# Kernel tuning notes

Hardware: AMD Instinct MI355X
Metric: run time of the kernel (lower is better)

The kernel has to match this reference:

```python
import jax, jax.numpy as jnp
import numpy as np
import math

N, E, D, H = 50000, 1600000, 128, 8
DH = D // H  # per-head dim
EPS = 1e-5   # batchnorm eps


def _attn(q_in, k_in, v_in, Wq, Wk, Wv, src, dst):
    # GAT-style edge attention: score = exp(clip(<K[src],Q[dst]>/sqrt(DH), -5, 5))
    Q = (q_in @ Wq.T).reshape(-1, H, DH)
    K = (k_in @ Wk.T).reshape(-1, H, DH)
    V = (v_in @ Wv.T).reshape(-1, H, DH)
    score = jnp.exp(jnp.clip((K[src] * Q[dst]).sum(-1) / math.sqrt(DH), -5.0, 5.0))  # [E,H]
    wV = jax.ops.segment_sum(V[src] * score[:, :, None], dst, num_segments=N)  # [N,H,DH]
    z = jax.ops.segment_sum(score, dst, num_segments=N)                         # [N,H]
    return (wV / z[:, :, None]).reshape(-1, D)


def _bn(x, gamma, beta):
    # BatchNorm1d in training mode: biased batch stats over nodes
    m = x.mean(0)
    v = x.var(0)
    return (x - m) / jnp.sqrt(v + EPS) * gamma + beta


def setup_inputs() -> dict:
    key = jax.random.key(0)
    ks = iter(jax.random.split(key, 48))

    def w(shape, scale=None):
        s = scale if scale is not None else 1.0 / math.sqrt(shape[-1])
        return jax.random.normal(next(ks), shape, jnp.float32) * s

    inp = dict(
        h=w((N, D), 1.0),
        sv=w((N, D), 1.0),
        src=jax.random.randint(next(ks), (E,), 0, N, jnp.int32),
        dst=jax.random.randint(next(ks), (E,), 0, N, jnp.int32),
    )
    for nm in ["Wq_sv", "Wk_sv", "Wv_sv", "Wq_cv", "Wk_cv", "Wv_cv",
               "Wq_sh", "Wk_sh", "Wv_sh"]:
        inp[nm] = w((D, D))
    inp.update(
        Wo=w((D, 2 * D)), bo=jnp.zeros((D,), jnp.float32),
        Wo_h=w((D, 2 * D)), bo_h=jnp.zeros((D,), jnp.float32),
        W1=w((2 * D, D)), b1=jnp.zeros((2 * D,), jnp.float32),
        W2=w((D, 2 * D)), b2=jnp.zeros((D,), jnp.float32),
        W1h=w((2 * D, D)), b1h=jnp.zeros((2 * D,), jnp.float32),
        W2h=w((D, 2 * D)), b2h=jnp.zeros((D,), jnp.float32),
        Wg1=w((D, D)), bg1=jnp.zeros((D,), jnp.float32),
        Wg2=w((D, D)), bg2=jnp.zeros((D,), jnp.float32),
        gbn1=jnp.ones((D,), jnp.float32), bbn1=jnp.zeros((D,), jnp.float32),
        gbn2=jnp.ones((D,), jnp.float32), bbn2=jnp.zeros((D,), jnp.float32),
        gbn1h=jnp.ones((D,), jnp.float32), bbn1h=jnp.zeros((D,), jnp.float32),
        gbn2h=jnp.ones((D,), jnp.float32), bbn2h=jnp.zeros((D,), jnp.float32),
    )
    return inp


def reference(h, sv, src, dst,
              Wq_sv, Wk_sv, Wv_sv, Wq_cv, Wk_cv, Wv_cv, Wq_sh, Wk_sh, Wv_sh,
              Wo, bo, Wo_h, bo_h,
              W1, b1, W2, b2, W1h, b1h, W2h, b2h,
              Wg1, bg1, Wg2, bg2,
              gbn1, bbn1, gbn2, bbn2, gbn1h, bbn1h, gbn2h, bbn2h):
    h_in1, sv_in1 = h, sv
    # --- h branch ---
    a_self = _attn(h, h, h, Wq_sv, Wk_sv, Wv_sv, src, dst)
    a_cross = _attn(h, sv, sv, Wq_cv, Wk_cv, Wv_cv, src, dst)
    hO = jnp.concatenate([a_self, a_cross], -1) @ Wo.T + bo
    h1 = _bn(h_in1 + hO, gbn1, bbn1)
    ffn = jax.nn.relu(h1 @ W1.T + b1) @ W2.T + b2
    h_out = _bn(h1 + ffn, gbn2, bbn2)
    # --- state-vector branch ---
    a_self_h = _attn(sv, sv, sv, Wq_sh, Wk_sh, Wv_sh, src, dst)
    # faithful to source: cross_attention_v weights reused here
    a_cross_h = _attn(sv, h_in1, h_in1, Wq_cv, Wk_cv, Wv_cv, src, dst)
    svO = jnp.concatenate([a_self_h, a_cross_h], -1) @ Wo_h.T + bo_h
    g1 = jax.nn.sigmoid(h_in1 @ Wg1.T + bg1)
    sv1 = _bn((1.0 - g1) * sv_in1 + g1 * svO, gbn1h, bbn1h)
    ffn_h = jax.nn.relu(sv1 @ W1h.T + b1h) @ W2h.T + b2h
    g2 = jax.nn.sigmoid(h_in1 @ Wg2.T + bg2)
    sv_out = _bn((1.0 - g2) * sv1 + g2 * ffn_h, gbn2h, bbn2h)
    return (h_out, sv_out)
```

## Files before the change

### kernel.cpp

```cpp
#include <hip/hip_runtime.h>

typedef _Float16 f16x8 __attribute__((ext_vector_type(8)));
typedef _Float16 f16x2 __attribute__((ext_vector_type(2)));
typedef __fp16 fp16x2_raw __attribute__((ext_vector_type(2)));
typedef float f32x4 __attribute__((ext_vector_type(4)));
typedef float f32x2 __attribute__((ext_vector_type(2)));
typedef unsigned int uint32;
typedef unsigned short ushort16;
typedef unsigned char uchar;

#define EPS_BN 1e-5f

__device__ __forceinline__ uint32 pk16(float a, float b){
  fp16x2_raw h = __builtin_amdgcn_cvt_pkrtz(a, b);
  return *(uint32*)&h;
}
__device__ __forceinline__ uchar f2fp8(float f){
  uint32 p = __builtin_amdgcn_cvt_pk_fp8_f32(f, f, 0, false);
  return (uchar)(p & 0xff);
}
__device__ __forceinline__ f32x2 fp8pair_lo(uint32 w){
  return __builtin_amdgcn_cvt_pk_f32_fp8(w, false);
}
__device__ __forceinline__ f32x2 fp8pair_hi(uint32 w){
  return __builtin_amdgcn_cvt_pk_f32_fp8(w, true);
}

struct WEnt { const float* s; const float* s2; ushort16* d; int KD, MD, nfrag; };
struct WConv { WEnt e[16]; };

__global__ __launch_bounds__(256) void conv_w_k(WConv a){
  WEnt t = a.e[blockIdx.y];
  int fid = blockIdx.x * 256 + threadIdx.x;
  if (fid >= t.nfrag) return;
  int lane = fid & 63, sm = fid >> 6;
  int MT = t.MD >> 4;
  int s = sm / MT, m = sm - s * MT;
  int row = m * 16 + (lane & 15);
  int col = s * 32 + (lane >> 4) * 8;
  const float* sp = t.s;
  if (t.s2 && row >= 128){ sp = t.s2; row -= 128; }
  const float* p = sp + (size_t)row * t.KD + col;
  uint4 o;
  o.x = pk16(p[0], p[1]); o.y = pk16(p[2], p[3]);
  o.z = pk16(p[4], p[5]); o.w = pk16(p[6], p[7]);
  *(uint4*)(t.d + (size_t)fid * 8) = o;
}

__global__ __launch_bounds__(256) void conv2h_k(const float* __restrict__ a, const float* __restrict__ b,
                                                ushort16* __restrict__ da, ushort16* __restrict__ db, int n,
                                                const int* __restrict__ dst, int* __restrict__ cnt, int E){
  if (blockIdx.y < 2){
    const float* s = blockIdx.y ? b : a;
    ushort16* d = blockIdx.y ? db : da;
    int i = (blockIdx.x * 256 + threadIdx.x) * 4;
    if (i >= n) return;
    float4 v = *(const float4*)(s + i);
    uint2 p;
    p.x = pk16(v.x, v.y);
    p.y = pk16(v.z, v.w);
    *(uint2*)(d + i) = p;
  } else {
    int i = blockIdx.x * 256 + threadIdx.x;
    int stride = gridDim.x * 256;
    for (; i < E; i += stride) atomicAdd(&cnt[dst[i]], 1);
  }
}

__global__ __launch_bounds__(256) void scan_part_k(const int* __restrict__ cnt, int* __restrict__ bsum, int N){
  int tid = threadIdx.x, lane = tid & 63, wv = tid >> 6;
  int base = blockIdx.x * 1024 + tid * 4;
  int ts = 0;
  #pragma unroll
  for (int j = 0; j < 4; j++) if (base + j < N) ts += cnt[base + j];
  #pragma unroll
  for (int d = 1; d < 64; d <<= 1) ts += __shfl_xor(ts, d);
  __shared__ int wt[4];
  if (lane == 0) wt[wv] = ts;
  __syncthreads();
  if (tid == 0) bsum[blockIdx.x] = wt[0] + wt[1] + wt[2] + wt[3];
}

__global__ __launch_bounds__(256) void scan_out_k(const int* __restrict__ cnt, const int* __restrict__ bsum,
                                                  int* __restrict__ row_off, int* __restrict__ cursor,
                                                  int* __restrict__ bcur,
                                                  int N, int E, int shift){
  int tid = threadIdx.x, lane = tid & 63, wv = tid >> 6;
  int bp = 0;
  for (int i = lane; i < (int)blockIdx.x; i += 64) bp += bsum[i];
  #pragma unroll
  for (int d = 1; d < 64; d <<= 1) bp += __shfl_xor(bp, d);
  int base = blockIdx.x * 1024 + tid * 4;
  int c[4]; int ts = 0;
  #pragma unroll
  for (int j = 0; j < 4; j++){ c[j] = (base + j < N) ? cnt[base + j] : 0; ts += c[j]; }
  int inc = ts;
  #pragma unroll
  for (int d = 1; d < 64; d <<= 1){
    int t = __shfl_up(inc, d);
    if (lane >= d) inc += t;
  }
  int wexcl = inc - ts;
  __shared__ int wt[4];
  if (lane == 63) wt[wv] = inc;
  __syncthreads();
  int woff = 0;
  for (int w = 0; w < 4; w++) if (w < wv) woff += wt[w];
  int off = bp + woff + wexcl;
  int mask = (1 << shift) - 1;
  #pragma unroll
  for (int j = 0; j < 4; j++){
    int d = base + j;
    if (d < N){
      row_off[d] = off; cursor[d] = off;
      if ((d & mask) == 0) bcur[d >> shift] = off;
      off += c[j];
    }
  }
  if (blockIdx.x == 0 && tid == 0) row_off[N] = E;
}

#define BIN_TB 512
#define BIN_TILE 4096
__global__ __launch_bounds__(512) void bin_k(const int* __restrict__ src, const int* __restrict__ dst,
                                             int* __restrict__ bcur, uint2* __restrict__ ebuf,
                                             int E, int shift, int B){
  __shared__ int lhist[128];
  __shared__ int lstart[128];
  __shared__ int gbase[128];
  __shared__ uint2 lpair[BIN_TILE];
  int tid = threadIdx.x;
  int base = blockIdx.x * BIN_TILE;
  int cnt = E - base; if (cnt > BIN_TILE) cnt = BIN_TILE;
  if (tid < 128) lhist[tid] = 0;
  __syncthreads();
  int myb[8], myrank[8];
  uint2 myp[8];
  int nmine = 0;
  #pragma unroll
  for (int j = 0; j < 8; j++){
    int i = tid + j * BIN_TB;
    if (i < cnt){
      int s = src[base + i], d = dst[base + i];
      int b = d >> shift;
      myp[nmine] = make_uint2((uint32)s, (uint32)d);
      myb[nmine] = b;
      myrank[nmine] = atomicAdd(&lhist[b], 1);
      nmine++;
    }
  }
  __syncthreads();
  if (tid == 0){
    int run = 0;
    for (int b = 0; b < B; b++){ lstart[b] = run; run += lhist[b]; }
  }
  __syncthreads();
  if (tid < B) gbase[tid] = atomicAdd(&bcur[tid], lhist[tid]);
  for (int j = 0; j < nmine; j++){
    lpair[lstart[myb[j]] + myrank[j]] = myp[j];
  }
  __syncthreads();
  for (int i = tid; i < cnt; i += BIN_TB){
    uint2 p = lpair[i];
    int b = (int)(p.y >> shift);
    ebuf[gbase[b] + (i - lstart[b])] = p;
  }
}

#define BF_SPLIT 8
__global__ __launch_bounds__(256) void bfill_k(const uint2* __restrict__ ebuf, const int* __restrict__ row_off,
                                               int* __restrict__ cursor, int* __restrict__ esrc,
                                               int shift, int N){
  int b = blockIdx.x / BF_SPLIT, slice = blockIdx.x % BF_SPLIT;
  int d0 = b << shift;
  int d1 = (b + 1) << shift; if (d1 > N) d1 = N;
  if (d0 >= N) return;
  int e0 = row_off[d0], e1 = row_off[d1];
  for (int i = e0 + slice * 256 + (int)threadIdx.x; i < e1; i += 256 * BF_SPLIT){
    uint2 p = ebuf[i];
    int pos = atomicAdd(&cursor[p.y], 1);
    esrc[pos] = (int)p.x;
  }
}

struct QkvArgs {
  const ushort16* Xq[4];
  const ushort16* Xkv[4];
  const ushort16* Wq[4];
  const ushort16* Wk[4];
  const ushort16* Wv[4];
  ushort16* Qo[4];
};
__global__ __launch_bounds__(256) void gemm_qkv_k(
    QkvArgs A, uchar* __restrict__ KV8, int N)
{
  __shared__ _Float16 Qs[4][16 * 136];
  __shared__ uchar Ks[4][16 * 136];
  __shared__ uchar Vs[4][16 * 136];
  int slot = blockIdx.y;
  int toff = slot << 8;
  const ushort16* Xq = A.Xq[slot];
  const ushort16* Xkv = A.Xkv[slot];
  ushort16* Qo = A.Qo[slot];
  int lane = threadIdx.x & 63, wv = threadIdx.x >> 6;
  int l15 = lane & 15, kq = lane >> 4;
  int rowbase = (blockIdx.x * 4 + wv) * 16;
  int row = rowbase + l15;
  int rc = row < N ? row : N - 1;
  const f16x8* aq = (const f16x8*)(Xq + (size_t)rc * 128 + kq * 8);
  const f16x8* ak = (const f16x8*)(Xkv + (size_t)rc * 128 + kq * 8);
  f16x8 Aq[4], Ak[4];
  #pragma unroll
  for (int s = 0; s < 4; s++){ Aq[s] = aq[s * 4]; Ak[s] = ak[s * 4]; }
  const f16x8* Wqf = (const f16x8*)A.Wq[slot];
  const f16x8* Wkf = (const f16x8*)A.Wk[slot];
  const f16x8* Wvf = (const f16x8*)A.Wv[slot];
  f32x4 q[8], k[8], v[8];
  #pragma unroll
  for (int m = 0; m < 8; m++){ q[m] = (f32x4)(0.f); k[m] = (f32x4)(0.f); v[m] = (f32x4)(0.f); }
  #pragma unroll
  for (int s = 0; s < 4; s++){
    #pragma unroll
    for (int m = 0; m < 8; m++){
      int fi = (s * 8 + m) * 64 + lane;
      q[m] = __builtin_amdgcn_mfma_f32_16x16x32_f16(Aq[s], Wqf[fi], q[m], 0, 0, 0);
      k[m] = __builtin_amdgcn_mfma_f32_16x16x32_f16(Ak[s], Wkf[fi], k[m], 0, 0, 0);
      v[m] = __builtin_amdgcn_mfma_f32_16x16x32_f16(Ak[s], Wvf[fi], v[m], 0, 0, 0);
    }
  }
  #pragma unroll
  for (int m = 0; m < 8; m++){
    int col = m * 16 + l15;
    #pragma unroll
    for (int r = 0; r < 4; r++){
      int lrow = kq * 4 + r;
      Qs[wv][lrow * 136 + col] = (_Float16)q[m][r];
      Ks[wv][lrow * 136 + col] = f2fp8(k[m][r]);
      Vs[wv][lrow * 136 + col] = f2fp8(v[m][r]);
    }
  }
  #pragma unroll
  for (int p = 0; p < 4; p++){
    int lrow = p * 4 + (lane >> 4);
    int rr = rowbase + lrow;
    int col8 = l15 * 8;
    if (rr < N){
      uint4 qv = *(uint4*)&Qs[wv][lrow * 136 + col8];
      *(uint4*)(Qo + (size_t)rr * 128 + col8) = qv;
      uint2 kv = *(uint2*)&Ks[wv][lrow * 136 + col8];
      *(uint2*)(KV8 + (size_t)rr * 1024 + toff + col8) = kv;
      uint2 vv = *(uint2*)&Vs[wv][lrow * 136 + col8];
      *(uint2*)(KV8 + (size_t)rr * 1024 + toff + 128 + col8) = vv;
    }
  }
}

template<int KD, int MD, int EPI, int ABN, int ST, int GS>
__device__ __forceinline__ void gemm_body(
    const ushort16* __restrict__ X, const ushort16* __restrict__ W,
    const float* __restrict__ bias, const float* __restrict__ bias2,
    const ushort16* __restrict__ resb, const ushort16* __restrict__ gatep,
    const float* __restrict__ rstats, const float* __restrict__ rg, const float* __restrict__ rb,
    const float* __restrict__ astats, const float* __restrict__ ag, const float* __restrict__ ab,
    ushort16* __restrict__ outb, float* __restrict__ stats_out, int N, float invN,
    _Float16* OsBase, float* sstB, float* sst2B)
{
  constexpr int KS = KD / 32;
  constexpr int MT = MD / 16;
  constexpr int LSTR = MD + 8;
  int lane = threadIdx.x & 63, wv = threadIdx.x >> 6;
  _Float16* OsW = OsBase + wv * 16 * LSTR;
  int l15 = lane & 15, kq = lane >> 4;
  int rowbase = (blockIdx.x * 4 + wv) * 16;
  int row = rowbase + l15;
  int rc = row < N ? row : N - 1;
  const f16x8* ap = (const f16x8*)(X + (size_t)rc * KD + kq * 8);
  f16x8 a[KS];
  #pragma unroll
  for (int s = 0; s < KS; s++) a[s] = ap[s * 4];
  if constexpr (ABN){
    #pragma unroll
    for (int s = 0; s < KS; s++){
      #pragma unroll
      for (int j = 0; j < 8; j++){
        int c = s * 32 + kq * 8 + j;
        float mm = astats[c] * invN;
        float var = astats[128 + c] * invN - mm * mm;
        float rs = rsqrtf(var + EPS_BN);
        float scc = rs * ag[c];
        float shh = ab[c] - mm * scc;
        a[s][j] = (_Float16)((float)a[s][j] * scc + shh);
      }
    }
  }
  const f16x8* Wf = (const f16x8*)W;
  f32x4 acc[MT];
  #pragma unroll
  for (int m = 0; m < MT; m++) acc[m] = (f32x4)(0.f);
  #pragma unroll
  for (int s = 0; s < KS; s++){
    #pragma unroll
    for (int m = 0; m < MT; m++){
      acc[m] = __builtin_amdgcn_mfma_f32_16x16x32_f16(a[s], Wf[(s * MT + m) * 64 + lane], acc[m], 0, 0, 0);
    }
  }
  float ps[MT], ps2[MT];
  if constexpr (ST){
    #pragma unroll
    for (int m = 0; m < MT; m++){ ps[m] = 0.f; ps2[m] = 0.f; }
  }
  int r0 = rowbase + kq * 4;
  #pragma unroll
  for (int m = 0; m < MT; m++){
    int col = m * 16 + l15;
    float bv;
    if (bias2 && col >= 128) bv = bias2[col - 128];
    else bv = bias[col];
    float sc = 0.f, sh = 0.f;
    if constexpr (EPI == 5 || EPI == 6){
      float mm = rstats[col] * invN;
      float var = rstats[128 + col] * invN - mm * mm;
      float rs = rsqrtf(var + EPS_BN);
      sc = rs * rg[col]; sh = rb[col] - mm * sc;
    }
    #pragma unroll
    for (int r = 0; r < 4; r++){
      int rr = r0 + r;
      float v;
      {
        int rrc = rr < N ? rr : N - 1;
        v = acc[m][r] + bv;
        if constexpr (EPI == 1) v = fmaxf(v, 0.f);
        if constexpr (EPI == 2) v = 1.f / (1.f + __expf(-v));
        if constexpr (EPI == 3){
          union { ushort16 u; _Float16 h; } cv; cv.u = resb[(size_t)rrc * 128 + col];
          v += (float)cv.h;
        }
        if constexpr (EPI == 5){
          union { ushort16 u; _Float16 h; } cv; cv.u = resb[(size_t)rrc * 128 + col];
          v += (float)cv.h * sc + sh;
        }
        if constexpr (EPI == 4 || EPI == 6){
          union { ushort16 u; _Float16 h; } gv; gv.u = gatep[(size_t)rrc * GS + col];
          union { ushort16 u; _Float16 h; } cv; cv.u = resb[(size_t)rrc * 128 + col];
          float g = (float)gv.h;
          float rv = (float)cv.h;
          if constexpr (EPI == 6) rv = rv * sc + sh;
          v = (1.f - g) * rv + g * v;
        }
      }
      OsW[(kq * 4 + r) * LSTR + col] = (_Float16)v;
      if constexpr (ST){
        if (rr < N){ ps[m] += v; ps2[m] += v * v; }
      }
    }
  }
  if constexpr (MD == 128){
    #pragma unroll
    for (int p = 0; p < 4; p++){
      int lrow = p * 4 + (lane >> 4);
      int rr = rowbase + lrow;
      int col8 = l15 * 8;
      if (rr < N){
        uint4 ov = *(uint4*)&OsW[lrow * LSTR + col8];
        *(uint4*)(outb + (size_t)rr * MD + col8) = ov;
      }
    }
  } else {
    #pragma unroll
    for (int p = 0; p < 8; p++){
      int lrow = p * 2 + (lane >> 5);
      int rr = rowbase + lrow;
      int col8 = (lane & 31) * 8;
      if (rr < N){
        uint4 ov = *(uint4*)&OsW[lrow * LSTR + col8];
        *(uint4*)(outb + (size_t)rr * MD + col8) = ov;
      }
    }
  }
  if constexpr (ST){
    #pragma unroll
    for (int m = 0; m < MT; m++){
      float s = ps[m], s2 = ps2[m];
      s  += __shfl_xor(s, 16);  s  += __shfl_xor(s, 32);
      s2 += __shfl_xor(s2, 16); s2 += __shfl_xor(s2, 32);
      if (lane < 16){ sstB[wv * 128 + m * 16 + l15] = s; sst2B[wv * 128 + m * 16 + l15] = s2; }
    }
    __syncthreads();
    int tid = threadIdx.x;
    if (tid < 128){
      atomicAdd(&stats_out[tid], sstB[tid] + sstB[128 + tid] + sstB[256 + tid] + sstB[384 + tid]);
    } else {
      int c = tid - 128;
      atomicAdd(&stats_out[tid], sst2B[c] + sst2B[128 + c] + sst2B[256 + c] + sst2B[384 + c]);
    }
  }
}

template<int KD, int MD, int EPI, int ABN, int ST, int GS>
__global__ __launch_bounds__(256) void gemm_k(
    const ushort16* __restrict__ X, const ushort16* __restrict__ W,
    const float* __restrict__ bias, const float* __restrict__ bias2,
    const ushort16* __restrict__ resb, const ushort16* __restrict__ gatep,
    const float* __restrict__ rstats, const float* __restrict__ rg, const float* __restrict__ rb,
    const float* __restrict__ astats, const float* __restrict__ ag, const float* __restrict__ ab,
    ushort16* __restrict__ outb, float* __restrict__ stats_out, int N, float invN)
{
  __shared__ _Float16 Os[4 * 16 * (MD + 8)];
  __shared__ float sst[512];
  __shared__ float sst2[512];
  gemm_body<KD, MD, EPI, ABN, ST, GS>(X, W, bias, bias2, resb, gatep, rstats, rg, rb,
                                      astats, ag, ab, outb, stats_out, N, invN, Os, sst, sst2);
}

struct GPairArgs {
  const ushort16* X[2]; const ushort16* W[2];
  const float* bias[2];
  const ushort16* resb[2]; const ushort16* gatep[2];
  const float* rstats[2]; const float* rg[2]; const float* rb[2];
  const float* astats[2]; const float* ag[2]; const float* ab[2];
  ushort16* outb[2]; float* stats_out[2];
};
template<int KD, int MD, int EPI0, int EPI1, int ABN, int ST, int GS>
__global__ __launch_bounds__(256) void gemm_pair_k(GPairArgs A, int N, float invN)
{
  __shared__ _Float16 Os[4 * 16 * (MD + 8)];
  __shared__ float sst[512];
  __shared__ float sst2[512];
  int y = blockIdx.y;
  if (y == 0){
    gemm_body<KD, MD, EPI0, ABN, ST, GS>(A.X[0], A.W[0], A.bias[0], nullptr, A.resb[0], A.gatep[0],
        A.rstats[0], A.rg[0], A.rb[0], A.astats[0], A.ag[0], A.ab[0],
        A.outb[0], A.stats_out[0], N, invN, Os, sst, sst2);
  } else {
    gemm_body<KD, MD, EPI1, ABN, ST, GS>(A.X[1], A.W[1], A.bias[1], nullptr, A.resb[1], A.gatep[1],
        A.rstats[1], A.rg[1], A.rb[1], A.astats[1], A.ag[1], A.ab[1],
        A.outb[1], A.stats_out[1], N, invN, Os, sst, sst2);
  }
}

__global__ __launch_bounds__(256) void attn4_k(
    const ushort16* __restrict__ Qa, const ushort16* __restrict__ Qb,
    const ushort16* __restrict__ Qc, const ushort16* __restrict__ Qd,
    const uchar* __restrict__ KV,
    const int* __restrict__ row_off, const int* __restrict__ esrc,
    ushort16* __restrict__ cat_h, ushort16* __restrict__ cat_sv, int N)
{
  int wv = threadIdx.x >> 6, lane = threadIdx.x & 63;
  int n = blockIdx.x * 4 + wv;
  if (n >= N) return;
  int g = lane >> 4, j = lane & 15;
  uint32 j8 = (uint32)j * 8u;
  const float QS = 0.25f * 1.44269504088896f;
  const float CL = 7.21347520444482f;
  const ushort16* Qp[4] = {Qa, Qb, Qc, Qd};
  f32x2 q[4][4];
  #pragma unroll
  for (int t = 0; t < 4; t++){
    uint4 u = *(const uint4*)(Qp[t] + (size_t)n * 128 + j8);
    f16x2 h0 = *(f16x2*)&u.x, h1 = *(f16x2*)&u.y;
    f16x2 h2 = *(f16x2*)&u.z, h3 = *(f16x2*)&u.w;
    q[t][0].x = (float)h0.x * QS; q[t][0].y = (float)h0.y * QS;
    q[t][1].x = (float)h1.x * QS; q[t][1].y = (float)h1.y * QS;
    q[t][2].x = (float)h2.x * QS; q[t][2].y = (float)h2.y * QS;
    q[t][3].x = (float)h3.x * QS; q[t][3].y = (float)h3.y * QS;
  }
  int e0 = row_off[n], e1 = row_off[n + 1];
  int itmax = (e1 - e0 + 3) >> 2;
  f32x2 ac[4][4];
  #pragma unroll
  for (int t = 0; t < 4; t++){
    #pragma unroll
    for (int r = 0; r < 4; r++) ac[t][r] = (f32x2)(0.f);
  }
  float z[4] = {0.f, 0.f, 0.f, 0.f};
  int e = e0 + g;
  int s = (e < e1) ? esrc[e] : -1;
  uint32 off = ((uint32)(s < 0 ? 0 : s) << 10) + j8;
  uint2 kc[4], vc[4];
  #pragma unroll
  for (int t = 0; t < 4; t++){
    kc[t] = *(const uint2*)(KV + off + t * 256);
    vc[t] = *(const uint2*)(KV + off + t * 256 + 128);
  }
  for (int it = 0; it < itmax; ++it){
    int e2 = e + 4;
    int s2 = (e2 < e1) ? esrc[e2] : -1;
    uint32 off2 = ((uint32)(s2 < 0 ? 0 : s2) << 10) + j8;
    uint2 kn[4], vn[4];
    #pragma unroll
    for (int t = 0; t < 4; t++){
      kn[t] = *(const uint2*)(KV + off2 + t * 256);
      vn[t] = *(const uint2*)(KV + off2 + t * 256 + 128);
    }
    if (s >= 0){
      #pragma unroll
      for (int t = 0; t < 4; t++){
        f32x2 k0 = fp8pair_lo(kc[t].x), k1 = fp8pair_hi(kc[t].x);
        f32x2 k2 = fp8pair_lo(kc[t].y), k3 = fp8pair_hi(kc[t].y);
        f32x2 dd = k0 * q[t][0] + k1 * q[t][1] + k2 * q[t][2] + k3 * q[t][3];
        float d = dd.x + dd.y;
        d += __shfl_xor(d, 1);
        float sc = __builtin_amdgcn_exp2f(__builtin_amdgcn_fmed3f(d, -CL, CL));
        f32x2 v0 = fp8pair_lo(vc[t].x), v1 = fp8pair_hi(vc[t].x);
        f32x2 v2 = fp8pair_lo(vc[t].y), v3 = fp8pair_hi(vc[t].y);
        f32x2 sv; sv.x = sc; sv.y = sc;
        ac[t][0] += sv * v0; ac[t][1] += sv * v1;
        ac[t][2] += sv * v2; ac[t][3] += sv * v3;
        z[t] += sc;
      }
    }
    e = e2; s = s2; off = off2;
    #pragma unroll
    for (int t = 0; t < 4; t++){ kc[t] = kn[t]; vc[t] = vn[t]; }
  }
  #pragma unroll
  for (int t = 0; t < 4; t++){
    #pragma unroll
    for (int r = 0; r < 4; r++){
      ac[t][r].x += __shfl_xor(ac[t][r].x, 16);
      ac[t][r].y += __shfl_xor(ac[t][r].y, 16);
      ac[t][r].x += __shfl_xor(ac[t][r].x, 32);
      ac[t][r].y += __shfl_xor(ac[t][r].y, 32);
    }
    z[t] += __shfl_xor(z[t], 16);
    z[t] += __shfl_xor(z[t], 32);
  }
  if (g == 0){
    size_t base = (size_t)n * 256 + j8;
    #pragma unroll
    for (int t = 0; t < 4; t++){
      float rz = __builtin_amdgcn_rcpf(z[t]);
      uint4 o;
      o.x = pk16(ac[t][0].x * rz, ac[t][0].y * rz);
      o.y = pk16(ac[t][1].x * rz, ac[t][1].y * rz);
      o.z = pk16(ac[t][2].x * rz, ac[t][2].y * rz);
      o.w = pk16(ac[t][3].x * rz, ac[t][3].y * rz);
      ushort16* dp = (t < 2) ? cat_h : cat_sv;
      *(uint4*)(dp + base + (t & 1) * 128) = o;
    }
  }
}

struct Bn2Args {
  const ushort16* x[2]; const float* stats[2];
  const float* g[2]; const float* b[2]; float* out[2];
};
__global__ __launch_bounds__(256) void bn2_k(Bn2Args A, int total4, float invN)
{
  int y = blockIdx.y;
  int i = blockIdx.x * 256 + threadIdx.x;
  if (i >= total4) return;
  const ushort16* x = A.x[y];
  const float* stats = A.stats[y];
  const float* gamma = A.g[y];
  const float* beta = A.b[y];
  float* outf = A.out[y];
  uint2 xp = *(const uint2*)(x + (size_t)i * 4);
  f16x2 x01 = *(f16x2*)&xp.x, x23 = *(f16x2*)&xp.y;
  float xv[4] = {(float)x01.x, (float)x01.y, (float)x23.x, (float)x23.y};
  int c0 = (i * 4) & 127;
  float o[4];
  #pragma unroll
  for (int j = 0; j < 4; j++){
    int c = c0 + j;
    float m = stats[c] * invN;
    float var = stats[128 + c] * invN - m * m;
    float rstd = rsqrtf(var + EPS_BN);
    o[j] = (xv[j] - m) * rstd * gamma[c] + beta[c];
  }
  *(float4*)(outf + (size_t)i * 4) = make_float4(o[0], o[1], o[2], o[3]);
}

extern "C" void kernel_launch(void* const* d_in, const int* in_sizes, int n_in,
                              void* d_out, int out_size, void* d_ws, size_t ws_size,
                              hipStream_t stream) {
  const float* h   = (const float*)d_in[0];
  const float* sv  = (const float*)d_in[1];
  const int* src   = (const int*)d_in[2];
  const int* dst   = (const int*)d_in[3];
  const int N = in_sizes[0] / 128;
  const int E = in_sizes[2];

  char* wsb = (char*)d_ws;
  size_t o = 0;
  auto take = [&](size_t bytes)->size_t{
    size_t r = o;
    o = (o + bytes + 255) & ~(size_t)255;
    return r;
  };
  size_t big = (size_t)E * 8;
  if (big < (size_t)N * 1024) big = (size_t)N * 1024;
  size_t cnt_off    = take((size_t)N * 4);
  size_t stats_off  = take(4 * 256 * 4);
  size_t rowoff_off = take((size_t)(N + 1) * 4);
  size_t cursor_off = take((size_t)N * 4);
  size_t bsum_off   = take(256 * 4);
  size_t bcur_off   = take(128 * 4);
  size_t esrc_off   = take((size_t)E * 4);
  size_t big_off    = take(big);
  size_t wpool_off  = take((size_t)376832 * 2);
  size_t hf_off     = take((size_t)N * 128 * 2);
  size_t svf_off    = take((size_t)N * 128 * 2);
  size_t cath_off   = take((size_t)N * 256 * 2);
  size_t catsv_off  = take((size_t)N * 256 * 2);
  size_t Q1_off     = take((size_t)N * 128 * 2);
  size_t Q2_off     = take((size_t)N * 128 * 2);
  size_t X1_off     = take((size_t)N * 128 * 2);
  size_t X2_off     = take((size_t)N * 128 * 2);
  size_t G_off      = take((size_t)N * 256 * 2);

  int*    cnt     = (int*)(wsb + cnt_off);
  float*  stats   = (float*)(wsb + stats_off);
  int*    row_off = (int*)(wsb + rowoff_off);
  int*    cursor  = (int*)(wsb + cursor_off);
  int*    bsum    = (int*)(wsb + bsum_off);
  int*    bcur    = (int*)(wsb + bcur_off);
  int*    esrc    = (int*)(wsb + esrc_off);
  uint2*  ebuf    = (uint2*)(wsb + big_off);
  uchar*  KVall   = (uchar*)(wsb + big_off);
  ushort16* wpool = (ushort16*)(wsb + wpool_off);
  ushort16* h_f   = (ushort16*)(wsb + hf_off);
  ushort16* sv_f  = (ushort16*)(wsb + svf_off);
  ushort16* cat_h = (ushort16*)(wsb + cath_off);
  ushort16* cat_sv= (ushort16*)(wsb + catsv_off);
  ushort16* Q1    = (ushort16*)(wsb + Q1_off);
  ushort16* Q2    = (ushort16*)(wsb + Q2_off);
  ushort16* Xb1   = (ushort16*)(wsb + X1_off);
  ushort16* Xb2   = (ushort16*)(wsb + X2_off);
  ushort16* Gbuf  = (ushort16*)(wsb + G_off);
  ushort16* Q3 = Xb1;
  ushort16* Q4 = Xb2;

  ushort16* Wq_sv = wpool + 0 * 16384;
  ushort16* Wk_sv = wpool + 1 * 16384;
  ushort16* Wv_sv = wpool + 2 * 16384;
  ushort16* Wq_cv = wpool + 3 * 16384;
  ushort16* Wk_cv = wpool + 4 * 16384;
  ushort16* Wv_cv = wpool + 5 * 16384;
  ushort16* Wq_sh = wpool + 6 * 16384;
  ushort16* Wk_sh = wpool + 7 * 16384;
  ushort16* Wv_sh = wpool + 8 * 16384;
  ushort16* Wgb   = wpool + 147456;
  ushort16* Wob   = wpool + 180224;
  ushort16* Wohb  = wpool + 212992;
  ushort16* W1b   = wpool + 245760;
  ushort16* W2b   = wpool + 278528;
  ushort16* W1hb  = wpool + 311296;
  ushort16* W2hb  = wpool + 344064;

  const float* bo   = (const float*)d_in[14];
  const float* bo_h = (const float*)d_in[16];
  const float* b1   = (const float*)d_in[18];
  const float* b2   = (const float*)d_in[20];
  const float* b1h  = (const float*)d_in[22];
  const float* b2h  = (const float*)d_in[24];
  const float* bg1  = (const float*)d_in[26];
  const float* bg2  = (const float*)d_in[28];
  const float* gbn1  = (const float*)d_in[29];
  const float* bbn1  = (const float*)d_in[30];
  const float* gbn2  = (const float*)d_in[31];
  const float* bbn2  = (const float*)d_in[32];
  const float* gbn1h = (const float*)d_in[33];
  const float* bbn1h = (const float*)d_in[34];
  const float* gbn2h = (const float*)d_in[35];
  const float* bbn2h = (const float*)d_in[36];

  float* out_h  = (float*)d_out;
  float* out_sv = out_h + (size_t)N * 128;

  (void)hipMemsetAsync(wsb, 0, stats_off + 4 * 256 * 4, stream);

  WConv wc;
  {
    auto set = [&](int i, int din, int din2, size_t dstoff, int KD, int MD){
      wc.e[i].s  = (const float*)d_in[din];
      wc.e[i].s2 = (din2 >= 0) ? (const float*)d_in[din2] : nullptr;
      wc.e[i].d  = wpool + dstoff;
      wc.e[i].KD = KD; wc.e[i].MD = MD;
      wc.e[i].nfrag = KD * MD / 8;
    };
    for (int i = 0; i < 9; i++) set(i, 4 + i, -1, (size_t)i * 16384, 128, 128);
    set(9,  25, 27, 147456, 128, 256);
    set(10, 13, -1, 180224, 256, 128);
    set(11, 15, -1, 212992, 256, 128);
    set(12, 17, -1, 245760, 128, 256);
    set(13, 19, -1, 278528, 256, 128);
    set(14, 21, -1, 311296, 128, 256);
    set(15, 23, -1, 344064, 256, 128);
  }
  conv_w_k<<<dim3(16, 16), 256, 0, stream>>>(wc);

  int nelem = N * 128;
  int CVB = (nelem / 4 + 255) / 256;
  conv2h_k<<<dim3(CVB, 3), 256, 0, stream>>>(h, sv, h_f, sv_f, nelem, dst, cnt, E);

  int shift = 9;
  while ((((N - 1) >> shift) + 1) > 128) shift++;
  const int B = ((N - 1) >> shift) + 1;

  const int NB = (N + 1023) / 1024;
  scan_part_k<<<NB, 256, 0, stream>>>(cnt, bsum, N);
  scan_out_k<<<NB, 256, 0, stream>>>(cnt, bsum, row_off, cursor, bcur, N, E, shift);
  bin_k<<<(E + BIN_TILE - 1) / BIN_TILE, BIN_TB, 0, stream>>>(src, dst, bcur, ebuf, E, shift, B);
  bfill_k<<<B * BF_SPLIT, 256, 0, stream>>>(ebuf, row_off, cursor, esrc, shift, N);

  const int GB = (N + 63) / 64;
  const int AB = (N + 3) / 4;
  const int T4 = nelem / 4;
  const int APB = (T4 + 255) / 256;
  const float invN = 1.f / (float)N;

  gemm_k<128,256,2,0,0,256><<<GB, 256, 0, stream>>>(h_f, Wgb, bg1, bg2, nullptr, nullptr,
      nullptr, nullptr, nullptr, nullptr, nullptr, nullptr, Gbuf, nullptr, N, invN);

  QkvArgs qa;
  qa.Xq[0] = h_f;  qa.Xkv[0] = h_f;  qa.Wq[0] = Wq_sv; qa.Wk[0] = Wk_sv; qa.Wv[0] = Wv_sv; qa.Qo[0] = Q1;
  qa.Xq[1] = h_f;  qa.Xkv[1] = sv_f; qa.Wq[1] = Wq_cv; qa.Wk[1] = Wk_cv; qa.Wv[1] = Wv_cv; qa.Qo[1] = Q2;
  qa.Xq[2] = sv_f; qa.Xkv[2] = sv_f; qa.Wq[2] = Wq_sh; qa.Wk[2] = Wk_sh; qa.Wv[2] = Wv_sh; qa.Qo[2] = Q3;
  qa.Xq[3] = sv_f; qa.Xkv[3] = h_f;  qa.Wq[3] = Wq_cv; qa.Wk[3] = Wk_cv; qa.Wv[3] = Wv_cv; qa.Qo[3] = Q4;
  gemm_qkv_k<<<dim3(GB, 4), 256, 0, stream>>>(qa, KVall, N);
  attn4_k<<<AB, 256, 0, stream>>>(Q1, Q2, Q3, Q4, KVall, row_off, esrc, cat_h, cat_sv, N);

  {
    GPairArgs A = {};
    A.X[0] = cat_h;  A.W[0] = Wob;  A.bias[0] = bo;   A.resb[0] = h_f;  A.gatep[0] = nullptr;
    A.outb[0] = Xb1; A.stats_out[0] = stats;
    A.X[1] = cat_sv; A.W[1] = Wohb; A.bias[1] = bo_h; A.resb[1] = sv_f; A.gatep[1] = Gbuf;
    A.outb[1] = Q1;  A.stats_out[1] = stats + 512;
    gemm_pair_k<256,128,3,4,0,1,256><<<dim3(GB, 2), 256, 0, stream>>>(A, N, invN);
  }
  {
    GPairArgs A = {};
    A.X[0] = Xb1; A.W[0] = W1b;  A.bias[0] = b1;
    A.astats[0] = stats;       A.ag[0] = gbn1;  A.ab[0] = bbn1;  A.outb[0] = cat_h;
    A.X[1] = Q1;  A.W[1] = W1hb; A.bias[1] = b1h;
    A.astats[1] = stats + 512; A.ag[1] = gbn1h; A.ab[1] = bbn1h; A.outb[1] = cat_sv;
    gemm_pair_k<128,256,1,1,1,0,256><<<dim3(GB, 2), 256, 0, stream>>>(A, N, invN);
  }
  {
    GPairArgs A = {};
    A.X[0] = cat_h;  A.W[0] = W2b;  A.bias[0] = b2;  A.resb[0] = Xb1;
    A.rstats[0] = stats;       A.rg[0] = gbn1;  A.rb[0] = bbn1;
    A.outb[0] = Xb2; A.stats_out[0] = stats + 256;
    A.X[1] = cat_sv; A.W[1] = W2hb; A.bias[1] = b2h; A.resb[1] = Q1;  A.gatep[1] = Gbuf + 128;
    A.rstats[1] = stats + 512; A.rg[1] = gbn1h; A.rb[1] = bbn1h;
    A.outb[1] = Q2;  A.stats_out[1] = stats + 768;
    gemm_pair_k<256,128,5,6,0,1,256><<<dim3(GB, 2), 256, 0, stream>>>(A, N, invN);
  }
  {
    Bn2Args A;
    A.x[0] = Xb2; A.stats[0] = stats + 256; A.g[0] = gbn2;  A.b[0] = bbn2;  A.out[0] = out_h;
    A.x[1] = Q2;  A.stats[1] = stats + 768; A.g[1] = gbn2h; A.b[1] = bbn2h; A.out[1] = out_sv;
    bn2_k<<<dim3(APB, 2), 256, 0, stream>>>(A, T4, invN);
  }
}
```

Before: 818.8 us.

## Merge prep kernels, build CSR per bucket in LDS, fuse gate GEMM into QKV

Folds the weight conversion, fp16 input conversion and destination counting into one prep kernel. Counting now happens per coarse bucket through shared-memory histograms, so the global per-node count and the two scan kernels go away. A new per-bucket csr_k computes row offsets and scatters src indices with LDS atomics, replacing the global-cursor atomics of bfill_k. The gate GEMM also runs as a fifth grid slice of the QKV kernel, which cuts several launches and global atomics at the cost of a serial single-thread bucket scan and 1024-thread blocks limited to B (at most 128) blocks.

```diff
diff --git a/kernel.cpp b/kernel.cpp
--- a/kernel.cpp
+++ b/kernel.cpp
@@ -29,30 +29,14 @@
 struct WEnt { const float* s; const float* s2; ushort16* d; int KD, MD, nfrag; };
 struct WConv { WEnt e[16]; };
 
-__global__ __launch_bounds__(256) void conv_w_k(WConv a){
-  WEnt t = a.e[blockIdx.y];
-  int fid = blockIdx.x * 256 + threadIdx.x;
-  if (fid >= t.nfrag) return;
-  int lane = fid & 63, sm = fid >> 6;
-  int MT = t.MD >> 4;
-  int s = sm / MT, m = sm - s * MT;
-  int row = m * 16 + (lane & 15);
-  int col = s * 32 + (lane >> 4) * 8;
-  const float* sp = t.s;
-  if (t.s2 && row >= 128){ sp = t.s2; row -= 128; }
-  const float* p = sp + (size_t)row * t.KD + col;
-  uint4 o;
-  o.x = pk16(p[0], p[1]); o.y = pk16(p[2], p[3]);
-  o.z = pk16(p[4], p[5]); o.w = pk16(p[6], p[7]);
-  *(uint4*)(t.d + (size_t)fid * 8) = o;
-}
-
-__global__ __launch_bounds__(256) void conv2h_k(const float* __restrict__ a, const float* __restrict__ b,
-                                                ushort16* __restrict__ da, ushort16* __restrict__ db, int n,
-                                                const int* __restrict__ dst, int* __restrict__ cnt, int E){
-  if (blockIdx.y < 2){
-    const float* s = blockIdx.y ? b : a;
-    ushort16* d = blockIdx.y ? db : da;
+__global__ __launch_bounds__(256) void prep_k(WConv wc,
+    const float* __restrict__ a, const float* __restrict__ b,
+    ushort16* __restrict__ da, ushort16* __restrict__ db, int n,
+    const int* __restrict__ dst, int* __restrict__ bcnt, int E, int shift){
+  int y = blockIdx.y;
+  if (y < 2){
+    const float* s = y ? b : a;
+    ushort16* d = y ? db : da;
     int i = (blockIdx.x * 256 + threadIdx.x) * 4;
     if (i >= n) return;
     float4 v = *(const float4*)(s + i);
@@ -60,64 +44,44 @@
     p.x = pk16(v.x, v.y);
     p.y = pk16(v.z, v.w);
     *(uint2*)(d + i) = p;
+  } else if (y == 2){
+    __shared__ int lh[128];
+    if (blockIdx.x >= 512) return;
+    int tid = threadIdx.x;
+    if (tid < 128) lh[tid] = 0;
+    __syncthreads();
+    int stride = 512 * 256;
+    for (int i = blockIdx.x * 256 + tid; i < E; i += stride)
+      atomicAdd(&lh[dst[i] >> shift], 1);
+    __syncthreads();
+    if (tid < 128 && lh[tid]) atomicAdd(&bcnt[tid], lh[tid]);
   } else {
-    int i = blockIdx.x * 256 + threadIdx.x;
-    int stride = gridDim.x * 256;
-    for (; i < E; i += stride) atomicAdd(&cnt[dst[i]], 1);
-  }
-}
-
-__global__ __launch_bounds__(256) void scan_part_k(const int* __restrict__ cnt, int* __restrict__ bsum, int N){
-  int tid = threadIdx.x, lane = tid & 63, wv = tid >> 6;
-  int base = blockIdx.x * 1024 + tid * 4;
-  int ts = 0;
-  #pragma unroll
-  for (int j = 0; j < 4; j++) if (base + j < N) ts += cnt[base + j];
-  #pragma unroll
-  for (int d = 1; d < 64; d <<= 1) ts += __shfl_xor(ts, d);
-  __shared__ int wt[4];
-  if (lane == 0) wt[wv] = ts;
-  __syncthreads();
-  if (tid == 0) bsum[blockIdx.x] = wt[0] + wt[1] + wt[2] + wt[3];
-}
-
-__global__ __launch_bounds__(256) void scan_out_k(const int* __restrict__ cnt, const int* __restrict__ bsum,
-                                                  int* __restrict__ row_off, int* __restrict__ cursor,
-                                                  int* __restrict__ bcur,
-                                                  int N, int E, int shift){
-  int tid = threadIdx.x, lane = tid & 63, wv = tid >> 6;
-  int bp = 0;
-  for (int i = lane; i < (int)blockIdx.x; i += 64) bp += bsum[i];
-  #pragma unroll
-  for (int d = 1; d < 64; d <<= 1) bp += __shfl_xor(bp, d);
-  int base = blockIdx.x * 1024 + tid * 4;
-  int c[4]; int ts = 0;
-  #pragma unroll
-  for (int j = 0; j < 4; j++){ c[j] = (base + j < N) ? cnt[base + j] : 0; ts += c[j]; }
-  int inc = ts;
-  #pragma unroll
-  for (int d = 1; d < 64; d <<= 1){
-    int t = __shfl_up(inc, d);
-    if (lane >= d) inc += t;
-  }
-  int wexcl = inc - ts;
-  __shared__ int wt[4];
-  if (lane == 63) wt[wv] = inc;
-  __syncthreads();
-  int woff = 0;
-  for (int w = 0; w < 4; w++) if (w < wv) woff += wt[w];
-  int off = bp + woff + wexcl;
-  int mask = (1 << shift) - 1;
-  #pragma unroll
-  for (int j = 0; j < 4; j++){
-    int d = base + j;
-    if (d < N){
-      row_off[d] = off; cursor[d] = off;
-      if ((d & mask) == 0) bcur[d >> shift] = off;
-      off += c[j];
-    }
-  }
-  if (blockIdx.x == 0 && tid == 0) row_off[N] = E;
+    if (blockIdx.x >= 256) return;
+    WEnt t = wc.e[blockIdx.x >> 4];
+    int fid = (blockIdx.x & 15) * 256 + threadIdx.x;
+    if (fid >= t.nfrag) return;
+    int lane = fid & 63, sm = fid >> 6;
+    int MT = t.MD >> 4;
+    int s = sm / MT, m = sm - s * MT;
+    int row = m * 16 + (lane & 15);
+    int col = s * 32 + (lane >> 4) * 8;
+    const float* sp = t.s;
+    if (t.s2 && row >= 128){ sp = t.s2; row -= 128; }
+    const float* p = sp + (size_t)row * t.KD + col;
+    uint4 o;
+    o.x = pk16(p[0], p[1]); o.y = pk16(p[2], p[3]);
+    o.z = pk16(p[4], p[5]); o.w = pk16(p[6], p[7]);
+    *(uint4*)(t.d + (size_t)fid * 8) = o;
+  }
+}
+
+__global__ __launch_bounds__(64) void bscan_k(const int* __restrict__ bcnt,
+    int* __restrict__ bstart, int* __restrict__ bcur, int B){
+  if (threadIdx.x == 0){
+    int run = 0;
+    for (int b = 0; b < B; b++){ bstart[b] = run; bcur[b] = run; run += bcnt[b]; }
+    bstart[B] = run;
+  }
 }
 
 #define BIN_TB 512
@@ -167,92 +131,56 @@
   }
 }
 
-#define BF_SPLIT 8
-__global__ __launch_bounds__(256) void bfill_k(const uint2* __restrict__ ebuf, const int* __restrict__ row_off,
-                                               int* __restrict__ cursor, int* __restrict__ esrc,
-                                               int shift, int N){
-  int b = blockIdx.x / BF_SPLIT, slice = blockIdx.x % BF_SPLIT;
+#define CSR_TB 1024
+__global__ __launch_bounds__(1024) void csr_k(const uint2* __restrict__ ebuf,
+    const int* __restrict__ bstart, int* __restrict__ row_off, int* __restrict__ esrc,
+    int shift, int N, int E, int B){
+  __shared__ int lc[4096];
+  __shared__ int lcur[4096];
+  __shared__ int wsum[16];
+  int b = blockIdx.x;
   int d0 = b << shift;
-  int d1 = (b + 1) << shift; if (d1 > N) d1 = N;
-  if (d0 >= N) return;
-  int e0 = row_off[d0], e1 = row_off[d1];
-  for (int i = e0 + slice * 256 + (int)threadIdx.x; i < e1; i += 256 * BF_SPLIT){
+  int nd = 1 << shift; if (d0 + nd > N) nd = N - d0;
+  if (nd <= 0) return;
+  int e0 = bstart[b], e1 = bstart[b + 1];
+  int tid = threadIdx.x, lane = tid & 63, wv = tid >> 6;
+  for (int j = tid; j < nd; j += CSR_TB){ lc[j] = 0; lcur[j] = 0; }
+  __syncthreads();
+  for (int i = e0 + tid; i < e1; i += CSR_TB){
+    atomicAdd(&lc[(int)ebuf[i].y - d0], 1);
+  }
+  __syncthreads();
+  int base4 = tid * 4;
+  int v0 = (base4 + 0 < nd) ? lc[base4 + 0] : 0;
+  int v1 = (base4 + 1 < nd) ? lc[base4 + 1] : 0;
+  int v2 = (base4 + 2 < nd) ? lc[base4 + 2] : 0;
+  int v3 = (base4 + 3 < nd) ? lc[base4 + 3] : 0;
+  int ts = v0 + v1 + v2 + v3;
+  int inc = ts;
+  #pragma unroll
+  for (int d = 1; d < 64; d <<= 1){
+    int t = __shfl_up(inc, d);
+    if (lane >= d) inc += t;
+  }
+  if (lane == 63) wsum[wv] = inc;
+  __syncthreads();
+  int woff = 0;
+  for (int w = 0; w < 16; w++) if (w < wv) woff += wsum[w];
+  int excl = woff + (inc - ts);
+  int o0 = excl, o1 = o0 + v0, o2 = o1 + v1, o3 = o2 + v2;
+  __syncthreads();
+  if (base4 + 0 < nd){ lc[base4 + 0] = o0; row_off[d0 + base4 + 0] = e0 + o0; }
+  if (base4 + 1 < nd){ lc[base4 + 1] = o1; row_off[d0 + base4 + 1] = e0 + o1; }
+  if (base4 + 2 < nd){ lc[base4 + 2] = o2; row_off[d0 + base4 + 2] = e0 + o2; }
+  if (base4 + 3 < nd){ lc[base4 + 3] = o3; row_off[d0 + base4 + 3] = e0 + o3; }
+  __syncthreads();
+  for (int i = e0 + tid; i < e1; i += CSR_TB){
     uint2 p = ebuf[i];
-    int pos = atomicAdd(&cursor[p.y], 1);
-    esrc[pos] = (int)p.x;
-  }
-}
-
-struct QkvArgs {
-  const ushort16* Xq[4];
-  const ushort16* Xkv[4];
-  const ushort16* Wq[4];
-  const ushort16* Wk[4];
-  const ushort16* Wv[4];
-  ushort16* Qo[4];
-};
-__global__ __launch_bounds__(256) void gemm_qkv_k(
-    QkvArgs A, uchar* __restrict__ KV8, int N)
-{
-  __shared__ _Float16 Qs[4][16 * 136];
-  __shared__ uchar Ks[4][16 * 136];
-  __shared__ uchar Vs[4][16 * 136];
-  int slot = blockIdx.y;
-  int toff = slot << 8;
-  const ushort16* Xq = A.Xq[slot];
-  const ushort16* Xkv = A.Xkv[slot];
-  ushort16* Qo = A.Qo[slot];
-  int lane = threadIdx.x & 63, wv = threadIdx.x >> 6;
-  int l15 = lane & 15, kq = lane >> 4;
-  int rowbase = (blockIdx.x * 4 + wv) * 16;
-  int row = rowbase + l15;
-  int rc = row < N ? row : N - 1;
-  const f16x8* aq = (const f16x8*)(Xq + (size_t)rc * 128 + kq * 8);
-  const f16x8* ak = (const f16x8*)(Xkv + (size_t)rc * 128 + kq * 8);
-  f16x8 Aq[4], Ak[4];
-  #pragma unroll
-  for (int s = 0; s < 4; s++){ Aq[s] = aq[s * 4]; Ak[s] = ak[s * 4]; }
-  const f16x8* Wqf = (const f16x8*)A.Wq[slot];
-  const f16x8* Wkf = (const f16x8*)A.Wk[slot];
-  const f16x8* Wvf = (const f16x8*)A.Wv[slot];
-  f32x4 q[8], k[8], v[8];
-  #pragma unroll
-  for (int m = 0; m < 8; m++){ q[m] = (f32x4)(0.f); k[m] = (f32x4)(0.f); v[m] = (f32x4)(0.f); }
-  #pragma unroll
-  for (int s = 0; s < 4; s++){
-    #pragma unroll
-    for (int m = 0; m < 8; m++){
-      int fi = (s * 8 + m) * 64 + lane;
-      q[m] = __builtin_amdgcn_mfma_f32_16x16x32_f16(Aq[s], Wqf[fi], q[m], 0, 0, 0);
-      k[m] = __builtin_amdgcn_mfma_f32_16x16x32_f16(Ak[s], Wkf[fi], k[m], 0, 0, 0);
-      v[m] = __builtin_amdgcn_mfma_f32_16x16x32_f16(Ak[s], Wvf[fi], v[m], 0, 0, 0);
-    }
-  }
-  #pragma unroll
-  for (int m = 0; m < 8; m++){
-    int col = m * 16 + l15;
-    #pragma unroll
-    for (int r = 0; r < 4; r++){
-      int lrow = kq * 4 + r;
-      Qs[wv][lrow * 136 + col] = (_Float16)q[m][r];
-      Ks[wv][lrow * 136 + col] = f2fp8(k[m][r]);
-      Vs[wv][lrow * 136 + col] = f2fp8(v[m][r]);
-    }
-  }
-  #pragma unroll
-  for (int p = 0; p < 4; p++){
-    int lrow = p * 4 + (lane >> 4);
-    int rr = rowbase + lrow;
-    int col8 = l15 * 8;
-    if (rr < N){
-      uint4 qv = *(uint4*)&Qs[wv][lrow * 136 + col8];
-      *(uint4*)(Qo + (size_t)rr * 128 + col8) = qv;
-      uint2 kv = *(uint2*)&Ks[wv][lrow * 136 + col8];
-      *(uint2*)(KV8 + (size_t)rr * 1024 + toff + col8) = kv;
-      uint2 vv = *(uint2*)&Vs[wv][lrow * 136 + col8];
-      *(uint2*)(KV8 + (size_t)rr * 1024 + toff + 128 + col8) = vv;
-    }
-  }
+    int d = (int)p.y - d0;
+    int r = atomicAdd(&lcur[d], 1);
+    esrc[e0 + lc[d] + r] = (int)p.x;
+  }
+  if (b == B - 1 && tid == 0) row_off[N] = E;
 }
 
 template<int KD, int MD, int EPI, int ABN, int ST, int GS>
@@ -397,20 +325,92 @@
   }
 }
 
-template<int KD, int MD, int EPI, int ABN, int ST, int GS>
-__global__ __launch_bounds__(256) void gemm_k(
-    const ushort16* __restrict__ X, const ushort16* __restrict__ W,
-    const float* __restrict__ bias, const float* __restrict__ bias2,
-    const ushort16* __restrict__ resb, const ushort16* __restrict__ gatep,
-    const float* __restrict__ rstats, const float* __restrict__ rg, const float* __restrict__ rb,
-    const float* __restrict__ astats, const float* __restrict__ ag, const float* __restrict__ ab,
-    ushort16* __restrict__ outb, float* __restrict__ stats_out, int N, float invN)
+struct QkvArgs {
+  const ushort16* Xq[4];
+  const ushort16* Xkv[4];
+  const ushort16* Wq[4];
+  const ushort16* Wk[4];
+  const ushort16* Wv[4];
+  ushort16* Qo[4];
+};
+__global__ __launch_bounds__(256) void qkvg_k(
+    QkvArgs A, uchar* __restrict__ KV8,
+    const ushort16* __restrict__ Xg, const ushort16* __restrict__ Wg,
+    const float* __restrict__ bg1, const float* __restrict__ bg2,
+    ushort16* __restrict__ Gout, int N, float invN)
 {
-  __shared__ _Float16 Os[4 * 16 * (MD + 8)];
-  __shared__ float sst[512];
-  __shared__ float sst2[512];
-  gemm_body<KD, MD, EPI, ABN, ST, GS>(X, W, bias, bias2, resb, gatep, rstats, rg, rb,
-                                      astats, ag, ab, outb, stats_out, N, invN, Os, sst, sst2);
+  __shared__ char smem[38144];
+  int slot = blockIdx.y;
+  if (slot == 4){
+    _Float16* Os = (_Float16*)smem;
+    float* sst  = (float*)(smem + 33792);
+    float* sst2 = (float*)(smem + 33792 + 2048);
+    gemm_body<128,256,2,0,0,256>(Xg, Wg, bg1, bg2, nullptr, nullptr,
+        nullptr, nullptr, nullptr, nullptr, nullptr, nullptr,
+        Gout, nullptr, N, invN, Os, sst, sst2);
+    return;
+  }
+  _Float16* Qs = (_Float16*)smem;
+  uchar* Ks = (uchar*)(smem + 17408);
+  uchar* Vs = (uchar*)(smem + 17408 + 8704);
+  int toff = slot << 8;
+  const ushort16* Xq = A.Xq[slot];
+  const ushort16* Xkv = A.Xkv[slot];
+  ushort16* Qo = A.Qo[slot];
+  int lane = threadIdx.x & 63, wv = threadIdx.x >> 6;
+  _Float16* QsW = Qs + wv * 16 * 136;
+  uchar* KsW = Ks + wv * 16 * 136;
+  uchar* VsW = Vs + wv * 16 * 136;
+  int l15 = lane & 15, kq = lane >> 4;
+  int rowbase = (blockIdx.x * 4 + wv) * 16;
+  int row = rowbase + l15;
+  int rc = row < N ? row : N - 1;
+  const f16x8* aq = (const f16x8*)(Xq + (size_t)rc * 128 + kq * 8);
+  const f16x8* ak = (const f16x8*)(Xkv + (size_t)rc * 128 + kq * 8);
+  f16x8 Aq[4], Ak[4];
+  #pragma unroll
+  for (int s = 0; s < 4; s++){ Aq[s] = aq[s * 4]; Ak[s] = ak[s * 4]; }
+  const f16x8* Wqf = (const f16x8*)A.Wq[slot];
+  const f16x8* Wkf = (const f16x8*)A.Wk[slot];
+  const f16x8* Wvf = (const f16x8*)A.Wv[slot];
+  f32x4 q[8], k[8], v[8];
+  #pragma unroll
+  for (int m = 0; m < 8; m++){ q[m] = (f32x4)(0.f); k[m] = (f32x4)(0.f); v[m] = (f32x4)(0.f); }
+  #pragma unroll
+  for (int s = 0; s < 4; s++){
+    #pragma unroll
+    for (int m = 0; m < 8; m++){
+      int fi = (s * 8 + m) * 64 + lane;
+      q[m] = __builtin_amdgcn_mfma_f32_16x16x32_f16(Aq[s], Wqf[fi], q[m], 0, 0, 0);
+      k[m] = __builtin_amdgcn_mfma_f32_16x16x32_f16(Ak[s], Wkf[fi], k[m], 0, 0, 0);
+      v[m] = __builtin_amdgcn_mfma_f32_16x16x32_f16(Ak[s], Wvf[fi], v[m], 0, 0, 0);
+    }
+  }
+  #pragma unroll
+  for (int m = 0; m < 8; m++){
+    int col = m * 16 + l15;
+    #pragma unroll
+    for (int r = 0; r < 4; r++){
+      int lrow = kq * 4 + r;
+      QsW[lrow * 136 + col] = (_Float16)q[m][r];
+      KsW[lrow * 136 + col] = f2fp8(k[m][r]);
+      VsW[lrow * 136 + col] = f2fp8(v[m][r]);
+    }
+  }
+  #pragma unroll
+  for (int p = 0; p < 4; p++){
+    int lrow = p * 4 + (lane >> 4);
+    int rr = rowbase + lrow;
+    int col8 = l15 * 8;
+    if (rr < N){
+      uint4 qv = *(uint4*)&QsW[lrow * 136 + col8];
+      *(uint4*)(Qo + (size_t)rr * 128 + col8) = qv;
+      uint2 kv = *(uint2*)&KsW[lrow * 136 + col8];
+      *(uint2*)(KV8 + (size_t)rr * 1024 + toff + col8) = kv;
+      uint2 vv = *(uint2*)&VsW[lrow * 136 + col8];
+      *(uint2*)(KV8 + (size_t)rr * 1024 + toff + 128 + col8) = vv;
+    }
+  }
 }
 
 struct GPairArgs {
@@ -591,12 +591,11 @@
   };
   size_t big = (size_t)E * 8;
   if (big < (size_t)N * 1024) big = (size_t)N * 1024;
-  size_t cnt_off    = take((size_t)N * 4);
+  size_t bcnt_off   = take(128 * 4);
   size_t stats_off  = take(4 * 256 * 4);
+  size_t bstart_off = take(132 * 4);
+  size_t bcur_off   = take(128 * 4);
   size_t rowoff_off = take((size_t)(N + 1) * 4);
-  size_t cursor_off = take((size_t)N * 4);
-  size_t bsum_off   = take(256 * 4);
-  size_t bcur_off   = take(128 * 4);
   size_t esrc_off   = take((size_t)E * 4);
   size_t big_off    = take(big);
   size_t wpool_off  = take((size_t)376832 * 2);
@@ -610,12 +609,11 @@
   size_t X2_off     = take((size_t)N * 128 * 2);
   size_t G_off      = take((size_t)N * 256 * 2);
 
-  int*    cnt     = (int*)(wsb + cnt_off);
+  int*    bcnt    = (int*)(wsb + bcnt_off);
   float*  stats   = (float*)(wsb + stats_off);
+  int*    bstart  = (int*)(wsb + bstart_off);
+  int*    bcur    = (int*)(wsb + bcur_off);
   int*    row_off = (int*)(wsb + rowoff_off);
-  int*    cursor  = (int*)(wsb + cursor_off);
-  int*    bsum    = (int*)(wsb + bsum_off);
-  int*    bcur    = (int*)(wsb + bcur_off);
   int*    esrc    = (int*)(wsb + esrc_off);
   uint2*  ebuf    = (uint2*)(wsb + big_off);
   uchar*  KVall   = (uchar*)(wsb + big_off);
@@ -689,21 +687,19 @@
     set(14, 21, -1, 311296, 128, 256);
     set(15, 23, -1, 344064, 256, 128);
   }
-  conv_w_k<<<dim3(16, 16), 256, 0, stream>>>(wc);
-
-  int nelem = N * 128;
-  int CVB = (nelem / 4 + 255) / 256;
-  conv2h_k<<<dim3(CVB, 3), 256, 0, stream>>>(h, sv, h_f, sv_f, nelem, dst, cnt, E);
 
   int shift = 9;
   while ((((N - 1) >> shift) + 1) > 128) shift++;
   const int B = ((N - 1) >> shift) + 1;
 
-  const int NB = (N + 1023) / 1024;
-  scan_part_k<<<NB, 256, 0, stream>>>(cnt, bsum, N);
-  scan_out_k<<<NB, 256, 0, stream>>>(cnt, bsum, row_off, cursor, bcur, N, E, shift);
+  int nelem = N * 128;
+  int CVB = (nelem / 4 + 255) / 256;
+  int PXB = CVB > 512 ? CVB : 512;
+  prep_k<<<dim3(PXB, 4), 256, 0, stream>>>(wc, h, sv, h_f, sv_f, nelem, dst, bcnt, E, shift);
+
+  bscan_k<<<1, 64, 0, stream>>>(bcnt, bstart, bcur, B);
   bin_k<<<(E + BIN_TILE - 1) / BIN_TILE, BIN_TB, 0, stream>>>(src, dst, bcur, ebuf, E, shift, B);
-  bfill_k<<<B * BF_SPLIT, 256, 0, stream>>>(ebuf, row_off, cursor, esrc, shift, N);
+  csr_k<<<B, CSR_TB, 0, stream>>>(ebuf, bstart, row_off, esrc, shift, N, E, B);
 
   const int GB = (N + 63) / 64;
   const int AB = (N + 3) / 4;
@@ -711,15 +707,12 @@
   const int APB = (T4 + 255) / 256;
   const float invN = 1.f / (float)N;
 
-  gemm_k<128,256,2,0,0,256><<<GB, 256, 0, stream>>>(h_f, Wgb, bg1, bg2, nullptr, nullptr,
-      nullptr, nullptr, nullptr, nullptr, nullptr, nullptr, Gbuf, nullptr, N, invN);
-
   QkvArgs qa;
   qa.Xq[0] = h_f;  qa.Xkv[0] = h_f;  qa.Wq[0] = Wq_sv; qa.Wk[0] = Wk_sv; qa.Wv[0] = Wv_sv; qa.Qo[0] = Q1;
   qa.Xq[1] = h_f;  qa.Xkv[1] = sv_f; qa.Wq[1] = Wq_cv; qa.Wk[1] = Wk_cv; qa.Wv[1] = Wv_cv; qa.Qo[1] = Q2;
   qa.Xq[2] = sv_f; qa.Xkv[2] = sv_f; qa.Wq[2] = Wq_sh; qa.Wk[2] = Wk_sh; qa.Wv[2] = Wv_sh; qa.Qo[2] = Q3;
   qa.Xq[3] = sv_f; qa.Xkv[3] = h_f;  qa.Wq[3] = Wq_cv; qa.Wk[3] = Wk_cv; qa.Wv[3] = Wv_cv; qa.Qo[3] = Q4;
-  gemm_qkv_k<<<dim3(GB, 4), 256, 0, stream>>>(qa, KVall, N);
+  qkvg_k<<<dim3(GB, 5), 256, 0, stream>>>(qa, KVall, h_f, Wgb, bg1, bg2, Gbuf, N, invN);
   attn4_k<<<AB, 256, 0, stream>>>(Q1, Q2, Q3, Q4, KVall, row_off, esrc, cat_h, cat_sv, N);
 
   {
```

Measured after the change: 736.1 us. 1.11x faster.
